# Kernel optimization log

Measured on AMD Instinct MI355X. Metric: run time of the kernel, lower is better.

Reference implementation:

```python
import jax, jax.numpy as jnp
import numpy as np

B, L, DIM = 8, 512, 8          # batch, seq len, raw channels (value dim D = 2*DIM = 16)
ET, HID, H = 128, 128, 2       # embed_time, hidden_size, num_heads
MAXLEN = 512
NEG = -1e9


def setup_inputs() -> dict:
    key = jax.random.key(0)
    ks = jax.random.split(key, 40)
    def n(i, shape, s=0.05):
        return jax.random.normal(ks[i], shape, jnp.float32) * s
    vals = jax.random.normal(ks[0], (B, L, DIM), jnp.float32)
    msk = (jax.random.uniform(ks[1], (B, L, DIM)) > 0.2).astype(jnp.float32)
    x = jnp.concatenate([vals, msk], -1)                      # (B, L, 2*DIM)
    time_steps = jax.random.uniform(ks[2], (B, L), jnp.float32)
    return {
        'x': x, 'time_steps': time_steps,
        # learned time embedding: Linear(1, ET-1) periodic + Linear(1,1)
        'w_per': n(3, (1, ET - 1)), 'b_per': n(4, (ET - 1,)),
        'w_lin': n(5, (1, 1)), 'b_lin': n(6, (1,)),
        # MultiTimeAttention projections
        'Wq_t': n(7, (ET, ET)), 'bq_t': n(8, (ET,)),
        'Wk_t': n(9, (ET, ET)), 'bk_t': n(10, (ET,)),
        'Wo_t': n(11, (2 * DIM * H, HID)), 'bo_t': n(12, (HID,)),
        'pos_emb': n(13, (MAXLEN + 1, HID)), 'cls_emb': n(14, (1, HID)),
        # transformer block (BERT-style post-LN encoder layer, d_ff=HID)
        'tWq': n(15, (HID, HID)), 'tbq': n(16, (HID,)),
        'tWk': n(17, (HID, HID)), 'tbk': n(18, (HID,)),
        'tWv': n(19, (HID, HID)), 'tbv': n(20, (HID,)),
        'tWo': n(21, (HID, HID)), 'tbo': n(22, (HID,)),
        'ln1_g': jnp.ones((HID,), jnp.float32), 'ln1_b': jnp.zeros((HID,), jnp.float32),
        'fW1': n(23, (HID, HID)), 'fb1': n(24, (HID,)),
        'fW2': n(25, (HID, HID)), 'fb2': n(26, (HID,)),
        'ln2_g': jnp.ones((HID,), jnp.float32), 'ln2_b': jnp.zeros((HID,), jnp.float32),
        # BertPooler
        'pW': n(27, (HID, HID)), 'pb': n(28, (HID,)),
    }


def _time_emb(tt, w_per, b_per, w_lin, b_lin):
    tt = tt[..., None]                                        # (B, L, 1)
    return jnp.concatenate([tt @ w_lin + b_lin, jnp.sin(tt @ w_per + b_per)], -1)


def _ln(x, g, b, eps=1e-5):
    m = x.mean(-1, keepdims=True)
    v = ((x - m) ** 2).mean(-1, keepdims=True)
    return (x - m) / jnp.sqrt(v + eps) * g + b


def _mta(q_emb, k_emb, value, mask, Wq, bq, Wk, bk, Wo, bo):
    # MultiTimeAttention: scores broadcast to value-channel axis, softmax over keys
    D = value.shape[-1]
    dk = ET // H
    def split(e, W, b):
        p = e @ W + b
        return p.reshape(e.shape[0], -1, H, dk).transpose(0, 2, 1, 3)
    q = split(q_emb, Wq, bq)                                  # (Bq, H, Lq, dk)
    k = split(k_emb, Wk, bk)                                  # (B,  H, Lk, dk)
    scores = jnp.matmul(q, k.swapaxes(-1, -2)) / jnp.sqrt(jnp.float32(dk))  # (B,H,Lq,Lk)
    s5 = jnp.where(mask[:, None, None, :, :] == 0, NEG, scores[..., None])  # (B,H,Lq,Lk,D)
    p = jax.nn.softmax(s5, axis=-2)
    out = jnp.einsum('bhqkd,bkd->bhqd', p, value)             # (B, H, Lq, D)
    Bv = value.shape[0]
    out = out.transpose(0, 2, 1, 3).reshape(Bv, -1, H * D)
    return out @ Wo + bo


def _tblock(x, tWq, tbq, tWk, tbk, tWv, tbv, tWo, tbo, ln1_g, ln1_b,
            fW1, fb1, fW2, fb2, ln2_g, ln2_b):
    Bq, Lq, _ = x.shape
    dk = HID // H
    def heads(W, b):
        return (x @ W + b).reshape(Bq, Lq, H, dk).transpose(0, 2, 1, 3)
    q, k, v = heads(tWq, tbq), heads(tWk, tbk), heads(tWv, tbv)
    a = jax.nn.softmax(jnp.matmul(q, k.swapaxes(-1, -2)) / jnp.sqrt(jnp.float32(dk)), -1)
    o = jnp.matmul(a, v).transpose(0, 2, 1, 3).reshape(Bq, Lq, HID) @ tWo + tbo
    x = _ln(x + o, ln1_g, ln1_b)
    f = jax.nn.relu(x @ fW1 + fb1) @ fW2 + fb2
    return _ln(x + f, ln2_g, ln2_b)


def reference(x, time_steps, w_per, b_per, w_lin, b_lin,
              Wq_t, bq_t, Wk_t, bk_t, Wo_t, bo_t, pos_emb, cls_emb,
              tWq, tbq, tWk, tbk, tWv, tbv, tWo, tbo, ln1_g, ln1_b,
              fW1, fb1, fW2, fb2, ln2_g, ln2_b, pW, pb):
    Bx = x.shape[0]
    mask_half = x[:, :, DIM:]
    mask = jnp.concatenate([mask_half, mask_half], -1)        # (B, L, 2*DIM)
    key_e = _time_emb(time_steps, w_per, b_per, w_lin, b_lin)
    tq_e = _time_emb(time_steps, w_per, b_per, w_lin, b_lin)  # query_time_steps=None -> same
    cls_t = jnp.linspace(0.0, 1.0, 128, dtype=jnp.float32)[None]
    cls_q_e = _time_emb(cls_t, w_per, b_per, w_lin, b_lin)    # (1, 128, ET)
    cls_out = _mta(cls_q_e, key_e, x, mask, Wq_t, bq_t, Wk_t, bk_t, Wo_t, bo_t)
    out = _mta(tq_e, key_e, x, mask, Wq_t, bq_t, Wk_t, bk_t, Wo_t, bo_t)
    tb = (tWq, tbq, tWk, tbk, tWv, tbv, tWo, tbo, ln1_g, ln1_b,
          fW1, fb1, fW2, fb2, ln2_g, ln2_b)
    cls_repr = jnp.broadcast_to(cls_emb[None, :, :], (Bx, 1, HID))
    # encode(cls_out, is_pooling=True), pooling='bert': no pos emb, take token 0
    h = _tblock(jnp.concatenate([cls_repr, cls_out], 1), *tb)
    cls_pooling = jnp.tanh(h[:, 0] @ pW + pb)                 # (B, HID)
    # encode(out, is_pooling=False) [pretrain path]: pos emb + transformer, drop CLS
    h2 = jnp.concatenate([cls_repr, out], 1)                  # (B, L+1, HID)
    h2 = h2 + pos_emb[:h2.shape[1]][None]
    h2 = _tblock(h2, *tb)
    last_hidden_state = h2[:, 1:]                             # (B, L, HID)
    return cls_pooling, last_hidden_state
```

## Files before the change

### kernel.cpp

```cpp
#include <hip/hip_runtime.h>
#include <hip/hip_bf16.h>
#include <math.h>


static constexpr int NM_ = 8 * 513;
static constexpr int NC_ = 8 * 129;
static constexpr int NT_ = NM_ + NC_;

using bf = __hip_bfloat16;
typedef __attribute__((ext_vector_type(8))) short bf16x8;
typedef __attribute__((ext_vector_type(4))) short bf16x4;
typedef __attribute__((ext_vector_type(4))) float floatx4;
typedef __attribute__((ext_vector_type(8))) unsigned short ushortx8;

__device__ __forceinline__ float wave_reduce_sum(float v) {
    #pragma unroll
    for (int off = 32; off >= 1; off >>= 1) v += __shfl_xor(v, off);
    return v;
}
__device__ __forceinline__ float wave_reduce_max(float v) {
    #pragma unroll
    for (int off = 32; off >= 1; off >>= 1) v = fmaxf(v, __shfl_xor(v, off));
    return v;
}
__device__ __forceinline__ float u2f(unsigned short u) {
    return __uint_as_float(((unsigned)u) << 16);
}
__device__ __forceinline__ unsigned short f2u(float f) {
    unsigned u = __float_as_uint(f);
    return (unsigned short)((u + 0x7FFF + ((u >> 16) & 1)) >> 16);
}
__device__ __forceinline__ bf16x8 join8(bf16x4 lo, bf16x4 hi) {
    return __builtin_shufflevector(lo, hi, 0, 1, 2, 3, 4, 5, 6, 7);
}
__device__ __forceinline__ float rdin(const void* p, int i, int flag) {
    return flag ? u2f(((const unsigned short*)p)[i]) : ((const float*)p)[i];
}

struct PrepAll {
    const void* src[32]; int n[32]; int dstoff[32];
    const void* wsrc[8]; unsigned short* wdst[8]; float wscale[8];
    const void* ts; const void* w_per; const void* b_per;
    const void* w_lin; const void* b_lin;
    unsigned short* key_e16;
    const unsigned short* det;
};
__global__ void prep_all_kernel(PrepAll a, float* dst) {
    int flag = (a.det[0] == 0x3F80u) ? 1 : 0;
    int blk = blockIdx.x, tid = threadIdx.x;
    if (blk < 8224) {
        int which = blk / 257, bi = blk - which * 257;
        int i = bi * 256 + tid;
        if (i < a.n[which]) dst[a.dstoff[which] + i] = rdin(a.src[which], i, flag);
    } else if (blk < 8736) {
        int p = blk - 8224;
        int m = p >> 6;
        int idx = (p & 63) * 256 + tid;
        int c = idx >> 9;
        int l = (idx >> 3) & 63;
        int j = idx & 7;
        int k = (c >> 3) * 32 + (l >> 4) * 8 + j;
        int n = (c & 7) * 16 + (l & 15);
        a.wdst[m][idx] = f2u(rdin(a.wsrc[m], k * 128 + n, flag) * a.wscale[m]);
    } else {
        int p = blk - 8736;
        int row = p * 2 + (tid >> 7), j = tid & 127;
        float t = (row < 4096) ? rdin(a.ts, row, flag)
                               : (float)(row - 4096) * (1.0f / 127.0f);
        float v;
        if (j == 0) v = t * rdin(a.w_lin, 0, flag) + rdin(a.b_lin, 0, flag);
        else        v = sinf(t * rdin(a.w_per, j - 1, flag) + rdin(a.b_per, j - 1, flag));
        a.key_e16[row * 128 + j] = f2u(v);
    }
}

struct GemmM {
    const void* A[3]; const unsigned short* W[3]; const float* bias[3];
    unsigned short* C[3];
    int M[3]; int act[3]; int abf[3]; float bscale[3];
};
__global__ void __launch_bounds__(256)
gemm_mfma_kernel(GemmM p) {
    int y = blockIdx.y;
    const unsigned short* Wsw = p.W[y];
    const float* bias = p.bias[y];
    unsigned short* C = p.C[y];
    int M = p.M[y], act = p.act[y], abf = p.abf[y];
    float bscale = p.bscale[y];
    int m0 = blockIdx.x * 16;
    if (m0 >= M) return;
    __shared__ unsigned short As[16][136];
    int tid = threadIdx.x;
    if (abf) {
        const unsigned short* A = (const unsigned short*)p.A[y];
        int r = tid >> 4, c0 = (tid & 15) * 8;
        ushortx8 v = {0, 0, 0, 0, 0, 0, 0, 0};
        if (m0 + r < M) v = *(const ushortx8*)(A + (size_t)(m0 + r) * 128 + c0);
        *(ushortx8*)&As[r][c0] = v;
    } else {
        const float* A = (const float*)p.A[y];
        int r = tid >> 4, c0 = (tid & 15) * 8;
        float4 v0 = make_float4(0.f, 0.f, 0.f, 0.f), v1 = v0;
        if (m0 + r < M) {
            v0 = *(const float4*)(A + (size_t)(m0 + r) * 128 + c0);
            v1 = *(const float4*)(A + (size_t)(m0 + r) * 128 + c0 + 4);
        }
        *(ushort4*)&As[r][c0] = make_ushort4(f2u(v0.x), f2u(v0.y), f2u(v0.z), f2u(v0.w));
        *(ushort4*)&As[r][c0 + 4] = make_ushort4(f2u(v1.x), f2u(v1.y), f2u(v1.z), f2u(v1.w));
    }
    __syncthreads();

    int wv = tid >> 6, lane = tid & 63;
    floatx4 acc0 = {0.f, 0.f, 0.f, 0.f}, acc1 = acc0;
    int am = lane & 15, aq = lane >> 4;
    #pragma unroll
    for (int ks = 0; ks < 4; ++ks) {
        bf16x8 af = *(bf16x8*)&As[am][ks * 32 + aq * 8];
        const unsigned short* base = Wsw + ((size_t)ks * 8 + 2 * wv) * 512 + lane * 8;
        bf16x8 b0 = *(const bf16x8*)(base);
        bf16x8 b1 = *(const bf16x8*)(base + 512);
        acc0 = __builtin_amdgcn_mfma_f32_16x16x32_bf16(af, b0, acc0, 0, 0, 0);
        acc1 = __builtin_amdgcn_mfma_f32_16x16x32_bf16(af, b1, acc1, 0, 0, 0);
    }
    int col = lane & 15, rowb = (lane >> 4) * 4;
    #pragma unroll
    for (int t = 0; t < 2; ++t) {
        floatx4 acc = t ? acc1 : acc0;
        int n = wv * 32 + t * 16 + col;
        float bv = bias[n] * bscale;
        #pragma unroll
        for (int rg = 0; rg < 4; ++rg) {
            int m = m0 + rowb + rg;
            if (m < M) {
                float o = acc[rg] + bv;
                if (act) o = fmaxf(o, 0.f);
                C[(size_t)m * 128 + n] = f2u(o);
            }
        }
    }
}

__global__ void __launch_bounds__(256)
gemm_mfma_ln_kernel(const unsigned short* A, const unsigned short* Wsw, const float* bias,
                    const float* resid, const float* gam, const float* bet,
                    float* C) {
    int m0 = blockIdx.x * 16;
    __shared__ unsigned short As[16][136];
    __shared__ float redS[4][4][4], redQ[4][4][4];
    __shared__ float smean[16], sinv[16];
    int tid = threadIdx.x;
    {
        int r = tid >> 4, c0 = (tid & 15) * 8;
        ushortx8 v = *(const ushortx8*)(A + (size_t)(m0 + r) * 128 + c0);
        *(ushortx8*)&As[r][c0] = v;
    }
    __syncthreads();

    int wv = tid >> 6, lane = tid & 63;
    floatx4 acc0 = {0.f, 0.f, 0.f, 0.f}, acc1 = acc0;
    int am = lane & 15, aq = lane >> 4;
    #pragma unroll
    for (int ks = 0; ks < 4; ++ks) {
        bf16x8 af = *(bf16x8*)&As[am][ks * 32 + aq * 8];
        const unsigned short* base = Wsw + ((size_t)ks * 8 + 2 * wv) * 512 + lane * 8;
        bf16x8 b0 = *(const bf16x8*)(base);
        bf16x8 b1 = *(const bf16x8*)(base + 512);
        acc0 = __builtin_amdgcn_mfma_f32_16x16x32_bf16(af, b0, acc0, 0, 0, 0);
        acc1 = __builtin_amdgcn_mfma_f32_16x16x32_bf16(af, b1, acc1, 0, 0, 0);
    }

    int col = lane & 15, g = lane >> 4, rowb = g * 4;
    float ov[2][4];
    #pragma unroll
    for (int t = 0; t < 2; ++t) {
        int n = wv * 32 + t * 16 + col;
        float bv = bias[n];
        floatx4 acc = t ? acc1 : acc0;
        #pragma unroll
        for (int rg = 0; rg < 4; ++rg)
            ov[t][rg] = acc[rg] + bv + resid[(size_t)(m0 + rowb + rg) * 128 + n];
    }
    #pragma unroll
    for (int rg = 0; rg < 4; ++rg) {
        float s = ov[0][rg] + ov[1][rg];
        float q = ov[0][rg] * ov[0][rg] + ov[1][rg] * ov[1][rg];
        #pragma unroll
        for (int off = 8; off >= 1; off >>= 1) {
            s += __shfl_xor(s, off);
            q += __shfl_xor(q, off);
        }
        if ((lane & 15) == 0) { redS[wv][g][rg] = s; redQ[wv][g][rg] = q; }
    }
    __syncthreads();
    if (tid < 16) {
        int gg = tid >> 2, rg = tid & 3;
        float s = redS[0][gg][rg] + redS[1][gg][rg] + redS[2][gg][rg] + redS[3][gg][rg];
        float q = redQ[0][gg][rg] + redQ[1][gg][rg] + redQ[2][gg][rg] + redQ[3][gg][rg];
        float mean = s * 0.0078125f;
        float var = q * 0.0078125f - mean * mean;
        smean[tid] = mean;
        sinv[tid] = rsqrtf(var + 1e-5f);
    }
    __syncthreads();
    #pragma unroll
    for (int t = 0; t < 2; ++t) {
        int n = wv * 32 + t * 16 + col;
        float gm = gam[n], bb = bet[n];
        #pragma unroll
        for (int rg = 0; rg < 4; ++rg) {
            int row = rowb + rg;
            C[(size_t)(m0 + row) * 128 + n] = (ov[t][rg] - smean[row]) * sinv[row] * gm + bb;
        }
    }
}

__global__ void __launch_bounds__(256)
ffn_ln_kernel(const float* x1, const unsigned short* W1, const float* b1,
              const unsigned short* W2, const float* b2,
              const float* gam, const float* bet, float* C) {
    int m0 = blockIdx.x * 16;
    __shared__ float Xs[16][128];
    __shared__ unsigned short As[16][136];
    __shared__ unsigned short Hs[16][136];
    __shared__ float redS[4][4][4], redQ[4][4][4];
    __shared__ float smean[16], sinv[16];
    int tid = threadIdx.x;
    {
        int r = tid >> 4, c0 = (tid & 15) * 8;
        float4 v0 = *(const float4*)(x1 + (size_t)(m0 + r) * 128 + c0);
        float4 v1 = *(const float4*)(x1 + (size_t)(m0 + r) * 128 + c0 + 4);
        *(float4*)&Xs[r][c0] = v0;
        *(float4*)&Xs[r][c0 + 4] = v1;
        *(ushort4*)&As[r][c0] = make_ushort4(f2u(v0.x), f2u(v0.y), f2u(v0.z), f2u(v0.w));
        *(ushort4*)&As[r][c0 + 4] = make_ushort4(f2u(v1.x), f2u(v1.y), f2u(v1.z), f2u(v1.w));
    }
    __syncthreads();

    int wv = tid >> 6, lane = tid & 63;
    int am = lane & 15, aq = lane >> 4;
    int col = lane & 15, g = lane >> 4, rowb = g * 4;

    {
        floatx4 acc0 = {0.f, 0.f, 0.f, 0.f}, acc1 = acc0;
        #pragma unroll
        for (int ks = 0; ks < 4; ++ks) {
            bf16x8 af = *(bf16x8*)&As[am][ks * 32 + aq * 8];
            const unsigned short* base = W1 + ((size_t)ks * 8 + 2 * wv) * 512 + lane * 8;
            bf16x8 bb0 = *(const bf16x8*)(base);
            bf16x8 bb1 = *(const bf16x8*)(base + 512);
            acc0 = __builtin_amdgcn_mfma_f32_16x16x32_bf16(af, bb0, acc0, 0, 0, 0);
            acc1 = __builtin_amdgcn_mfma_f32_16x16x32_bf16(af, bb1, acc1, 0, 0, 0);
        }
        #pragma unroll
        for (int t = 0; t < 2; ++t) {
            int n = wv * 32 + t * 16 + col;
            float bv = b1[n];
            floatx4 acc = t ? acc1 : acc0;
            #pragma unroll
            for (int rg = 0; rg < 4; ++rg)
                Hs[rowb + rg][n] = f2u(fmaxf(acc[rg] + bv, 0.f));
        }
    }
    __syncthreads();

    floatx4 acc0 = {0.f, 0.f, 0.f, 0.f}, acc1 = acc0;
    #pragma unroll
    for (int ks = 0; ks < 4; ++ks) {
        bf16x8 af = *(bf16x8*)&Hs[am][ks * 32 + aq * 8];
        const unsigned short* base = W2 + ((size_t)ks * 8 + 2 * wv) * 512 + lane * 8;
        bf16x8 bb0 = *(const bf16x8*)(base);
        bf16x8 bb1 = *(const bf16x8*)(base + 512);
        acc0 = __builtin_amdgcn_mfma_f32_16x16x32_bf16(af, bb0, acc0, 0, 0, 0);
        acc1 = __builtin_amdgcn_mfma_f32_16x16x32_bf16(af, bb1, acc1, 0, 0, 0);
    }
    float ov[2][4];
    #pragma unroll
    for (int t = 0; t < 2; ++t) {
        int n = wv * 32 + t * 16 + col;
        float bv = b2[n];
        floatx4 acc = t ? acc1 : acc0;
        #pragma unroll
        for (int rg = 0; rg < 4; ++rg)
            ov[t][rg] = acc[rg] + bv + Xs[rowb + rg][n];
    }
    #pragma unroll
    for (int rg = 0; rg < 4; ++rg) {
        float s = ov[0][rg] + ov[1][rg];
        float q = ov[0][rg] * ov[0][rg] + ov[1][rg] * ov[1][rg];
        #pragma unroll
        for (int off = 8; off >= 1; off >>= 1) {
            s += __shfl_xor(s, off);
            q += __shfl_xor(q, off);
        }
        if ((lane & 15) == 0) { redS[wv][g][rg] = s; redQ[wv][g][rg] = q; }
    }
    __syncthreads();
    if (tid < 16) {
        int gg = tid >> 2, rg = tid & 3;
        float s = redS[0][gg][rg] + redS[1][gg][rg] + redS[2][gg][rg] + redS[3][gg][rg];
        float q = redQ[0][gg][rg] + redQ[1][gg][rg] + redQ[2][gg][rg] + redQ[3][gg][rg];
        float mean = s * 0.0078125f;
        float var = q * 0.0078125f - mean * mean;
        smean[tid] = mean;
        sinv[tid] = rsqrtf(var + 1e-5f);
    }
    __syncthreads();
    #pragma unroll
    for (int t = 0; t < 2; ++t) {
        int n = wv * 32 + t * 16 + col;
        float gm = gam[n], bb = bet[n];
        #pragma unroll
        for (int rg = 0; rg < 4; ++rg) {
            int row = rowb + rg;
            C[(size_t)(m0 + row) * 128 + n] = (ov[t][rg] - smean[row]) * sinv[row] * gm + bb;
        }
    }
}

__global__ void mta_out_assemble_kernel(const float* att, const float* W, const float* bias,
                                        const float* cls_emb, const float* pos, float* xin) {
    int tid = threadIdx.x;
    if (blockIdx.x == 320) {
        for (int e = tid; e < 16 * 128; e += 256) {
            int i = e >> 7, j = e & 127;
            int b = i >> 1;
            if ((i & 1) == 0) xin[(size_t)(b * 513) * 128 + j] = cls_emb[j] + pos[j];
            else              xin[(size_t)(4104 + b * 129) * 128 + j] = cls_emb[j];
        }
        return;
    }
    int m0 = blockIdx.x * 16;
    __shared__ float As[16][36];
    int r = tid >> 4, gq = tid & 15, c0 = gq * 8;
    if (gq < 2) {
        const float* src = att + (size_t)(m0 + r) * 32 + gq * 16;
        *(float4*)&As[r][gq * 16]      = *(const float4*)(src);
        *(float4*)&As[r][gq * 16 + 4]  = *(const float4*)(src + 4);
        *(float4*)&As[r][gq * 16 + 8]  = *(const float4*)(src + 8);
        *(float4*)&As[r][gq * 16 + 12] = *(const float4*)(src + 12);
    }
    __syncthreads();
    float acc[8];
    #pragma unroll
    for (int j = 0; j < 8; ++j) acc[j] = bias[c0 + j];
    #pragma unroll 8
    for (int k = 0; k < 32; ++k) {
        float a = As[r][k];
        const float4 w0 = *(const float4*)(W + (size_t)k * 128 + c0);
        const float4 w1 = *(const float4*)(W + (size_t)k * 128 + c0 + 4);
        acc[0] = fmaf(a, w0.x, acc[0]); acc[1] = fmaf(a, w0.y, acc[1]);
        acc[2] = fmaf(a, w0.z, acc[2]); acc[3] = fmaf(a, w0.w, acc[3]);
        acc[4] = fmaf(a, w1.x, acc[4]); acc[5] = fmaf(a, w1.y, acc[5]);
        acc[6] = fmaf(a, w1.z, acc[6]); acc[7] = fmaf(a, w1.w, acc[7]);
    }
    int m = m0 + r;
    size_t dstrow;
    if (m < 1024) {
        int b = m >> 7, rr = m & 127;
        dstrow = (size_t)(4104 + b * 129 + 1 + rr);
    } else {
        int mm = m - 1024;
        int b = mm >> 9, rr = mm & 511;
        dstrow = (size_t)(b * 513 + 1 + rr);
        const float* pr = pos + (size_t)(1 + rr) * 128 + c0;
        float4 p0 = *(const float4*)(pr);
        float4 p1 = *(const float4*)(pr + 4);
        acc[0] += p0.x; acc[1] += p0.y; acc[2] += p0.z; acc[3] += p0.w;
        acc[4] += p1.x; acc[5] += p1.y; acc[6] += p1.z; acc[7] += p1.w;
    }
    *(float4*)(xin + dstrow * 128 + c0) = make_float4(acc[0], acc[1], acc[2], acc[3]);
    *(float4*)(xin + dstrow * 128 + c0 + 4) = make_float4(acc[4], acc[5], acc[6], acc[7]);
}

__global__ void __launch_bounds__(256)
mta_att_kernel(const unsigned short* qp_cls, const unsigned short* qp_main,
               const unsigned short* kp, const float* x,
               float* att_cls, float* att_mn) {
    int is_cls = (blockIdx.x >= 32);
    int qt = is_cls ? (blockIdx.x - 32) : blockIdx.x;
    int h = blockIdx.y, b = blockIdx.z;
    int tid = threadIdx.x, lane = tid & 63, wv = tid >> 6;
    __shared__ unsigned short Qs[16][72];
    __shared__ unsigned short KV[64][72];
    __shared__ unsigned short sp[16][520];
    float* xv = (float*)&KV[0][0];
    int q0 = qt * 16;

    if (tid < 128) {
        int r = tid >> 3, c0 = (tid & 7) * 8;
        const unsigned short* qrow = is_cls ? (qp_cls + (size_t)(q0 + r) * 128 + h * 64)
                                            : (qp_main + (size_t)(b * 512 + q0 + r) * 128 + h * 64);
        *(ushortx8*)&Qs[r][c0] = *(const ushortx8*)(qrow + c0);
    }
    __syncthreads();

    bf16x8 qf0, qf1;
    {
        int m = lane & 15, g = lane >> 4;
        qf0 = *(const bf16x8*)&Qs[m][g * 8];
        qf1 = *(const bf16x8*)&Qs[m][32 + g * 8];
    }

    for (int kt = 0; kt < 8; ++kt) {
        int k0 = kt * 64;
        {
            int kk = tid >> 3, e0 = (tid & 7) * 8;
            #pragma unroll
            for (int it = 0; it < 2; ++it, kk += 32)
                *(ushortx8*)&KV[kk][e0] =
                    *(const ushortx8*)(kp + (size_t)(b * 512 + k0 + kk) * 128 + h * 64 + e0);
        }
        __syncthreads();
        int kn = lane & 15, g = lane >> 4;
        floatx4 acc = {0.f, 0.f, 0.f, 0.f};
        {
            bf16x8 b0 = *(const bf16x8*)&KV[wv * 16 + kn][g * 8];
            acc = __builtin_amdgcn_mfma_f32_16x16x32_bf16(qf0, b0, acc, 0, 0, 0);
            bf16x8 b1 = *(const bf16x8*)&KV[wv * 16 + kn][32 + g * 8];
            acc = __builtin_amdgcn_mfma_f32_16x16x32_bf16(qf1, b1, acc, 0, 0, 0);
        }
        int colk = k0 + wv * 16 + kn;
        #pragma unroll
        for (int rg = 0; rg < 4; ++rg) sp[g * 4 + rg][colk] = f2u(acc[rg]);
        __syncthreads();
    }

    for (int rr = wv; rr < 16; rr += 4) {
        float m = -1e30f;
        for (int k = lane; k < 512; k += 64) m = fmaxf(m, u2f(sp[rr][k]));
        m = wave_reduce_max(m);
        for (int k = lane; k < 512; k += 64) sp[rr][k] = f2u(expf(u2f(sp[rr][k]) - m));
    }

    int d = lane >> 3, sub = lane & 7;
    int qb = wv * 4;
    float num[4] = {0.f, 0.f, 0.f, 0.f}, den[4] = {0.f, 0.f, 0.f, 0.f};
    for (int kt = 0; kt < 8; ++kt) {
        int k0 = kt * 64;
        __syncthreads();
        {
            int kk = tid >> 2, c0 = (tid & 3) * 4;
            float4 v = *(const float4*)(x + (size_t)(b * 512 + k0 + kk) * 16 + c0);
            xv[kk * 17 + c0] = v.x; xv[kk * 17 + c0 + 1] = v.y;
            xv[kk * 17 + c0 + 2] = v.z; xv[kk * 17 + c0 + 3] = v.w;
        }
        __syncthreads();
        #pragma unroll
        for (int i = 0; i < 8; ++i) {
            int kk = sub + 8 * i;
            float mk = xv[kk * 17 + 8 + d];
            float vv = xv[kk * 17 + d];
            #pragma unroll
            for (int q = 0; q < 4; ++q) {
                float em = u2f(sp[qb + q][k0 + kk]) * mk;
                den[q] += em;
                num[q] = fmaf(em, vv, num[q]);
            }
        }
    }
    #pragma unroll
    for (int q = 0; q < 4; ++q) {
        #pragma unroll
        for (int off2 = 4; off2 >= 1; off2 >>= 1) {
            num[q] += __shfl_xor(num[q], off2);
            den[q] += __shfl_xor(den[q], off2);
        }
        if (sub == 0) {
            int row = q0 + qb + q;
            float* dst = is_cls ? (att_cls + (size_t)(b * 128 + row) * 32)
                                : (att_mn + (size_t)(b * 512 + row) * 32);
            dst[h * 16 + d] = num[q] / den[q];
            dst[h * 16 + 8 + d] = 1.0f;
        }
    }
}

__global__ void __launch_bounds__(256)
tb_att_kernel(const unsigned short* qp, const unsigned short* kp,
              const unsigned short* vp, unsigned short* outp) {
    int is_cls = (blockIdx.x >= 33);
    int qt = is_cls ? blockIdx.x - 33 : blockIdx.x;
    int h = blockIdx.y, b = blockIdx.z;
    int Lq = is_cls ? 129 : 513;
    int base = is_cls ? (4104 + b * 129) : (b * 513);
    int nkt = is_cls ? 3 : 9;
    int tid = threadIdx.x, lane = tid & 63, wv = tid >> 6;
    __shared__ unsigned short Qs[16][72];
    __shared__ unsigned short KV[64][72];
    __shared__ unsigned short sp[16][588];
    __shared__ float rinv[16];
    int q0 = qt * 16;

    if (tid < 128) {
        int r = tid >> 3, c0 = (tid & 7) * 8;
        int qr = q0 + r;
        ushortx8 v = {0, 0, 0, 0, 0, 0, 0, 0};
        if (qr < Lq) v = *(const ushortx8*)(qp + (size_t)(base + qr) * 128 + h * 64 + c0);
        *(ushortx8*)&Qs[r][c0] = v;
    }
    __syncthreads();

    bf16x8 qf0, qf1;
    {
        int m = lane & 15, g = lane >> 4;
        qf0 = *(const bf16x8*)&Qs[m][g * 8];
        qf1 = *(const bf16x8*)&Qs[m][32 + g * 8];
    }

    for (int kt = 0; kt < nkt; ++kt) {
        int k0 = kt * 64;
        {
            int kk = tid >> 3, e0 = (tid & 7) * 8;
            #pragma unroll
            for (int it = 0; it < 2; ++it, kk += 32) {
                int krow = k0 + kk;
                ushortx8 v = {0, 0, 0, 0, 0, 0, 0, 0};
                if (krow < Lq) v = *(const ushortx8*)(kp + (size_t)(base + krow) * 128 + h * 64 + e0);
                *(ushortx8*)&KV[kk][e0] = v;
            }
        }
        __syncthreads();
        int kn = lane & 15, g = lane >> 4;
        floatx4 acc = {0.f, 0.f, 0.f, 0.f};
        {
            bf16x8 b0 = *(const bf16x8*)&KV[wv * 16 + kn][g * 8];
            acc = __builtin_amdgcn_mfma_f32_16x16x32_bf16(qf0, b0, acc, 0, 0, 0);
            bf16x8 b1 = *(const bf16x8*)&KV[wv * 16 + kn][32 + g * 8];
            acc = __builtin_amdgcn_mfma_f32_16x16x32_bf16(qf1, b1, acc, 0, 0, 0);
        }
        int colk = k0 + wv * 16 + kn;
        #pragma unroll
        for (int rg = 0; rg < 4; ++rg)
            sp[g * 4 + rg][colk] = f2u((colk < Lq) ? acc[rg] : -1e30f);
        __syncthreads();
    }

    int kend = nkt * 64;
    for (int rr = wv; rr < 16; rr += 4) {
        float m = -1e30f;
        for (int k = lane; k < kend; k += 64) m = fmaxf(m, u2f(sp[rr][k]));
        m = wave_reduce_max(m);
        float sum = 0.f;
        for (int k = lane; k < kend; k += 64) {
            float e = expf(u2f(sp[rr][k]) - m);
            sp[rr][k] = f2u(e);
            sum += e;
        }
        sum = wave_reduce_sum(sum);
        if (lane == 0) rinv[rr] = 1.f / sum;
    }

    floatx4 oacc = {0.f, 0.f, 0.f, 0.f};
    for (int kt = 0; kt < nkt; ++kt) {
        int k0 = kt * 64;
        __syncthreads();
        {
            int kk = tid & 31, e0 = (tid >> 5) * 8;
            #pragma unroll
            for (int it = 0; it < 2; ++it, kk += 32) {
                int krow = k0 + kk;
                ushortx8 v = {0, 0, 0, 0, 0, 0, 0, 0};
                if (krow < Lq) v = *(const ushortx8*)(vp + (size_t)(base + krow) * 128 + h * 64 + e0);
                #pragma unroll
                for (int j = 0; j < 8; ++j) KV[e0 + j][kk] = v[j];
            }
        }
        __syncthreads();
        int dn = lane & 15, g = lane >> 4;
        #pragma unroll
        for (int c = 0; c < 2; ++c) {
            bf16x4 plo = *(const bf16x4*)&sp[lane & 15][k0 + c * 32 + g * 8];
            bf16x4 phi = *(const bf16x4*)&sp[lane & 15][k0 + c * 32 + g * 8 + 4];
            bf16x8 vf = *(const bf16x8*)&KV[wv * 16 + dn][c * 32 + g * 8];
            oacc = __builtin_amdgcn_mfma_f32_16x16x32_bf16(join8(plo, phi), vf, oacc, 0, 0, 0);
        }
    }
    int dcol = wv * 16 + (lane & 15), g = lane >> 4;
    #pragma unroll
    for (int rg = 0; rg < 4; ++rg) {
        int q = g * 4 + rg;
        int qr = q0 + q;
        if (qr < Lq)
            outp[(size_t)(base + qr) * 128 + h * 64 + dcol] = f2u(oacc[rg] * rinv[q]);
    }
}

__global__ void pool_gemm_kernel(const float* A, int lda, const float* W, const float* bias,
                                 float* C) {
    __shared__ float As[8][132];
    int tid = threadIdx.x;
    int r = tid >> 5, g = tid & 31;
    for (int c = g; c < 128; c += 32) As[r][c] = A[(size_t)r * lda + c];
    __syncthreads();
    int rr = tid >> 5, c0 = (tid & 31) * 4;
    float acc[4];
    #pragma unroll
    for (int j = 0; j < 4; ++j) acc[j] = bias[c0 + j];
    for (int k = 0; k < 128; ++k) {
        float a = As[rr][k];
        const float4 w0 = *(const float4*)(W + (size_t)k * 128 + c0);
        acc[0] = fmaf(a, w0.x, acc[0]); acc[1] = fmaf(a, w0.y, acc[1]);
        acc[2] = fmaf(a, w0.z, acc[2]); acc[3] = fmaf(a, w0.w, acc[3]);
    }
    *(float4*)(C + (size_t)rr * 128 + c0) = make_float4(acc[0], acc[1], acc[2], acc[3]);
}

__global__ void finalize_kernel(const float* clsraw, const float* h2, float* out, int total) {
    int idx = blockIdx.x * 256 + threadIdx.x;
    if (idx >= total) return;
    float v;
    if (idx < 1024) {
        v = tanhf(clsraw[idx]);
    } else {
        int t = idx - 1024;
        int b = t >> 16;
        int rem = t & 65535;
        int i = rem >> 7, j = rem & 127;
        v = h2[((size_t)(b * 513 + 1 + i)) * 128 + j];
    }
    out[idx] = v;
}

extern "C" void kernel_launch(void* const* d_in, const int* in_sizes, int n_in,
                              void* d_out, int out_size, void* d_ws, size_t ws_size,
                              hipStream_t stream) {
    float* w = (float*)d_ws;
    size_t off = 0;
    auto alloc = [&](size_t n) {
        float* p = w + off;
        off += (n + 3) & ~(size_t)3;
        return p;
    };
    auto allocU = [&](size_t n) { return (unsigned short*)alloc((n + 1) / 2); };

    PrepAll pa{};
    int nn = n_in < 32 ? n_in : 32;
    float* fin[32];
    for (int i = 0; i < nn; ++i) {
        pa.src[i] = d_in[i];
        pa.n[i] = in_sizes[i];
        fin[i] = alloc(in_sizes[i]);
        pa.dstoff[i] = (int)(fin[i] - w);
    }
    for (int i = nn; i < 32; ++i) { pa.src[i] = nullptr; pa.n[i] = 0; pa.dstoff[i] = 0; }

    const float* x       = fin[0];
    const float* bq_t    = fin[7];
    const float* bk_t    = fin[9];
    const float* Wo_t    = fin[10]; const float* bo_t = fin[11];
    const float* pos_emb = fin[12]; const float* cls_emb = fin[13];
    const float* tbq = fin[15]; const float* tbk = fin[17]; const float* tbv = fin[19];
    const float* tbo = fin[21];
    const float* ln1_g = fin[22]; const float* ln1_b = fin[23];
    const float* fb1 = fin[25]; const float* fb2 = fin[27];
    const float* ln2_g = fin[28]; const float* ln2_b = fin[29];
    const float* pW = fin[30]; const float* pb = fin[31];

    const int widx[8] = {8, 6, 14, 16, 18, 20, 24, 26};
    unsigned short* wsw[8];
    for (int i = 0; i < 8; ++i) {
        wsw[i] = allocU(16384);
        pa.wsrc[i] = d_in[widx[i]];
        pa.wdst[i] = wsw[i];
        pa.wscale[i] = (i == 1 || i == 2) ? 0.125f : 1.0f;
    }
    pa.ts = d_in[1]; pa.w_per = d_in[2]; pa.b_per = d_in[3];
    pa.w_lin = d_in[4]; pa.b_lin = d_in[5];
    pa.det = (const unsigned short*)d_in[22];

    unsigned short* key_e16 = allocU(4224 * 128);
    unsigned short* cls_e16 = key_e16 + 4096 * 128;
    pa.key_e16 = key_e16;

    unsigned short* qp_main16 = allocU(4096 * 128);
    unsigned short* kp_main16 = allocU(4096 * 128);
    unsigned short* qp_cls16  = allocU(128 * 128);
    float* att_all = alloc(5120 * 32);
    float* att_cls = att_all;
    float* att_mn  = att_all + 1024 * 32;
    float* xin     = alloc((size_t)NT_ * 128);
    unsigned short* tbq16 = allocU((size_t)NT_ * 128);
    unsigned short* tbk16 = allocU((size_t)NT_ * 128);
    unsigned short* tbv16 = allocU((size_t)NT_ * 128);
    unsigned short* tba16 = allocU((size_t)NT_ * 128);
    float* tb_x1   = alloc((size_t)NT_ * 128);
    float* x2      = alloc((size_t)NT_ * 128);
    float* clsraw  = alloc(8 * 128);
    (void)ws_size;

    prep_all_kernel<<<10848, 256, 0, stream>>>(pa, w);

    {
        GemmM p{};
        p.A[0] = key_e16; p.W[0] = wsw[0]; p.bias[0] = bk_t; p.C[0] = kp_main16;
        p.M[0] = 4096; p.act[0] = 0; p.abf[0] = 1; p.bscale[0] = 1.f;
        p.A[1] = key_e16; p.W[1] = wsw[1]; p.bias[1] = bq_t; p.C[1] = qp_main16;
        p.M[1] = 4096; p.act[1] = 0; p.abf[1] = 1; p.bscale[1] = 0.125f;
        p.A[2] = cls_e16; p.W[2] = wsw[1]; p.bias[2] = bq_t; p.C[2] = qp_cls16;
        p.M[2] = 128; p.act[2] = 0; p.abf[2] = 1; p.bscale[2] = 0.125f;
        gemm_mfma_kernel<<<dim3(256, 3), 256, 0, stream>>>(p);
    }

    mta_att_kernel<<<dim3(40, 2, 8), 256, 0, stream>>>(qp_cls16, qp_main16, kp_main16,
                                                       x, att_cls, att_mn);

    mta_out_assemble_kernel<<<321, 256, 0, stream>>>(att_all, Wo_t, bo_t, cls_emb, pos_emb, xin);

    {
        GemmM p{};
        const unsigned short* Ws[3] = {wsw[2], wsw[3], wsw[4]};
        const float* bs[3] = {tbq, tbk, tbv};
        unsigned short* Cs[3] = {tbq16, tbk16, tbv16};
        float sc[3] = {0.125f, 1.f, 1.f};
        for (int y = 0; y < 3; ++y) {
            p.A[y] = xin; p.W[y] = Ws[y]; p.bias[y] = bs[y]; p.C[y] = Cs[y];
            p.M[y] = NT_; p.act[y] = 0; p.abf[y] = 0; p.bscale[y] = sc[y];
        }
        gemm_mfma_kernel<<<dim3((NT_ + 15) / 16, 3), 256, 0, stream>>>(p);
    }

    tb_att_kernel<<<dim3(42, 2, 8), 256, 0, stream>>>(tbq16, tbk16, tbv16, tba16);

    gemm_mfma_ln_kernel<<<NT_ / 16, 256, 0, stream>>>(tba16, wsw[5], tbo, xin, ln1_g, ln1_b, tb_x1);

    ffn_ln_kernel<<<NT_ / 16, 256, 0, stream>>>(tb_x1, wsw[6], fb1, wsw[7], fb2, ln2_g, ln2_b, x2);

    pool_gemm_kernel<<<1, 256, 0, stream>>>(x2 + (size_t)4104 * 128, 129 * 128, pW, pb, clsraw);

    finalize_kernel<<<(out_size + 255) / 256, 256, 0, stream>>>(clsraw, x2, (float*)d_out, out_size);
}
```

Measured before the change: 202.5 us.

## Fuse output scatter into FFN-LN, MFMA att-value reduction, skip unused input copies

The FFN+LayerNorm kernel now writes the last hidden state straight into the output buffer and stores only the CLS rows needed for pooling. The pooler applies tanh itself, so the finalize kernel and the full x2 buffer are dropped. The MTA attention value/mask weighted sum becomes a bf16 MFMA over a staged masked-value matrix instead of scalar loops with shuffles. The prep kernel also skips fp32 copies of inputs never read in fp32. Together this removes one launch and a large copy pass but lowers the precision of the attention numerator and denominator to bf16.

```diff
diff --git a/kernel.cpp b/kernel.cpp
--- a/kernel.cpp
+++ b/kernel.cpp
@@ -38,7 +38,7 @@
 }
 
 struct PrepAll {
-    const void* src[32]; int n[32]; int dstoff[32];
+    const void* src[32]; int n[32]; int dstoff[32]; int conv[32];
     const void* wsrc[8]; unsigned short* wdst[8]; float wscale[8];
     const void* ts; const void* w_per; const void* b_per;
     const void* w_lin; const void* b_lin;
@@ -50,6 +50,7 @@
     int blk = blockIdx.x, tid = threadIdx.x;
     if (blk < 8224) {
         int which = blk / 257, bi = blk - which * 257;
+        if (!a.conv[which]) return;
         int i = bi * 256 + tid;
         if (i < a.n[which]) dst[a.dstoff[which] + i] = rdin(a.src[which], i, flag);
     } else if (blk < 8736) {
@@ -217,7 +218,7 @@
 __global__ void __launch_bounds__(256)
 ffn_ln_kernel(const float* x1, const unsigned short* W1, const float* b1,
               const unsigned short* W2, const float* b2,
-              const float* gam, const float* bet, float* C) {
+              const float* gam, const float* bet, float* dout, float* x2c) {
     int m0 = blockIdx.x * 16;
     __shared__ float Xs[16][128];
     __shared__ unsigned short As[16][136];
@@ -312,7 +313,17 @@
         #pragma unroll
         for (int rg = 0; rg < 4; ++rg) {
             int row = rowb + rg;
-            C[(size_t)(m0 + row) * 128 + n] = (ov[t][rg] - smean[row]) * sinv[row] * gm + bb;
+            int m = m0 + row;
+            float val = (ov[t][rg] - smean[row]) * sinv[row] * gm + bb;
+            if (m < NM_) {
+                int b = m / 513, r = m - b * 513;
+                if (r >= 1)
+                    dout[1024 + (size_t)b * 65536 + (size_t)(r - 1) * 128 + n] = val;
+            } else {
+                int mc = m - NM_;
+                int b = mc / 129, r = mc - b * 129;
+                if (r == 0) x2c[b * 128 + n] = val;
+            }
         }
     }
 }
@@ -383,6 +394,7 @@
     __shared__ unsigned short Qs[16][72];
     __shared__ unsigned short KV[64][72];
     __shared__ unsigned short sp[16][520];
+    __shared__ unsigned short Bt[16][520];
     float* xv = (float*)&KV[0][0];
     int q0 = qt * 16;
 
@@ -432,9 +444,6 @@
         for (int k = lane; k < 512; k += 64) sp[rr][k] = f2u(expf(u2f(sp[rr][k]) - m));
     }
 
-    int d = lane >> 3, sub = lane & 7;
-    int qb = wv * 4;
-    float num[4] = {0.f, 0.f, 0.f, 0.f}, den[4] = {0.f, 0.f, 0.f, 0.f};
     for (int kt = 0; kt < 8; ++kt) {
         int k0 = kt * 64;
         __syncthreads();
@@ -445,33 +454,52 @@
             xv[kk * 17 + c0 + 2] = v.z; xv[kk * 17 + c0 + 3] = v.w;
         }
         __syncthreads();
-        #pragma unroll
-        for (int i = 0; i < 8; ++i) {
-            int kk = sub + 8 * i;
-            float mk = xv[kk * 17 + 8 + d];
-            float vv = xv[kk * 17 + d];
+        {
+            int c = tid & 15, k4 = (tid >> 4) * 4;
             #pragma unroll
-            for (int q = 0; q < 4; ++q) {
-                float em = u2f(sp[qb + q][k0 + kk]) * mk;
-                den[q] += em;
-                num[q] = fmaf(em, vv, num[q]);
+            for (int i = 0; i < 4; ++i) {
+                int k = k4 + i;
+                float val = (c < 8) ? xv[k * 17 + c] * xv[k * 17 + 8 + c]
+                                    : xv[k * 17 + c];
+                Bt[c][k0 + k] = f2u(val);
             }
         }
     }
-    #pragma unroll
-    for (int q = 0; q < 4; ++q) {
-        #pragma unroll
-        for (int off2 = 4; off2 >= 1; off2 >>= 1) {
-            num[q] += __shfl_xor(num[q], off2);
-            den[q] += __shfl_xor(den[q], off2);
-        }
-        if (sub == 0) {
-            int row = q0 + qb + q;
-            float* dst = is_cls ? (att_cls + (size_t)(b * 128 + row) * 32)
-                                : (att_mn + (size_t)(b * 512 + row) * 32);
-            dst[h * 16 + d] = num[q] / den[q];
-            dst[h * 16 + 8 + d] = 1.0f;
-        }
+    __syncthreads();
+
+    floatx4 macc = {0.f, 0.f, 0.f, 0.f};
+    {
+        int mq = lane & 15, g = lane >> 4;
+        #pragma unroll
+        for (int cc = 0; cc < 4; ++cc) {
+            int koff = (wv + cc * 4) * 32;
+            bf16x8 af = *(const bf16x8*)&sp[mq][koff + g * 8];
+            bf16x8 bfv = *(const bf16x8*)&Bt[mq][koff + g * 8];
+            macc = __builtin_amdgcn_mfma_f32_16x16x32_bf16(af, bfv, macc, 0, 0, 0);
+        }
+    }
+    float* redC = (float*)&KV[0][0];
+    float* Cfull = redC + 1024;
+    #pragma unroll
+    for (int rg = 0; rg < 4; ++rg) redC[(wv * 64 + lane) * 4 + rg] = macc[rg];
+    __syncthreads();
+    {
+        int l = tid >> 2, rg = tid & 3;
+        float s = redC[l * 4 + rg] + redC[(64 + l) * 4 + rg]
+                + redC[(128 + l) * 4 + rg] + redC[(192 + l) * 4 + rg];
+        int row = (l >> 4) * 4 + rg, c = l & 15;
+        Cfull[row * 16 + c] = s;
+    }
+    __syncthreads();
+    if (tid < 128) {
+        int r = tid >> 3, c = tid & 7;
+        float num = Cfull[r * 16 + c];
+        float den = Cfull[r * 16 + 8 + c];
+        int row = q0 + r;
+        float* dst = is_cls ? (att_cls + (size_t)(b * 128 + row) * 32)
+                            : (att_mn + (size_t)(b * 512 + row) * 32);
+        dst[h * 16 + c] = num / den;
+        dst[h * 16 + 8 + c] = 1.0f;
     }
 }
 
@@ -585,12 +613,12 @@
     }
 }
 
-__global__ void pool_gemm_kernel(const float* A, int lda, const float* W, const float* bias,
-                                 float* C) {
+__global__ void pool_tanh_kernel(const float* x2c, const float* W, const float* bias,
+                                 float* dout) {
     __shared__ float As[8][132];
     int tid = threadIdx.x;
     int r = tid >> 5, g = tid & 31;
-    for (int c = g; c < 128; c += 32) As[r][c] = A[(size_t)r * lda + c];
+    for (int c = g; c < 128; c += 32) As[r][c] = x2c[(size_t)r * 128 + c];
     __syncthreads();
     int rr = tid >> 5, c0 = (tid & 31) * 4;
     float acc[4];
@@ -602,23 +630,8 @@
         acc[0] = fmaf(a, w0.x, acc[0]); acc[1] = fmaf(a, w0.y, acc[1]);
         acc[2] = fmaf(a, w0.z, acc[2]); acc[3] = fmaf(a, w0.w, acc[3]);
     }
-    *(float4*)(C + (size_t)rr * 128 + c0) = make_float4(acc[0], acc[1], acc[2], acc[3]);
-}
-
-__global__ void finalize_kernel(const float* clsraw, const float* h2, float* out, int total) {
-    int idx = blockIdx.x * 256 + threadIdx.x;
-    if (idx >= total) return;
-    float v;
-    if (idx < 1024) {
-        v = tanhf(clsraw[idx]);
-    } else {
-        int t = idx - 1024;
-        int b = t >> 16;
-        int rem = t & 65535;
-        int i = rem >> 7, j = rem & 127;
-        v = h2[((size_t)(b * 513 + 1 + i)) * 128 + j];
-    }
-    out[idx] = v;
+    *(float4*)(dout + (size_t)rr * 128 + c0) =
+        make_float4(tanhf(acc[0]), tanhf(acc[1]), tanhf(acc[2]), tanhf(acc[3]));
 }
 
 extern "C" void kernel_launch(void* const* d_in, const int* in_sizes, int n_in,
@@ -636,13 +649,16 @@
     PrepAll pa{};
     int nn = n_in < 32 ? n_in : 32;
     float* fin[32];
+    const int needconv[32] = {1,0,0,0,0,0, 0,1, 0,1, 1,1, 1,1, 0,1, 0,1, 0,1,
+                              0,1, 1,1, 0,1, 0,1, 1,1, 1,1};
     for (int i = 0; i < nn; ++i) {
         pa.src[i] = d_in[i];
         pa.n[i] = in_sizes[i];
         fin[i] = alloc(in_sizes[i]);
         pa.dstoff[i] = (int)(fin[i] - w);
-    }
-    for (int i = nn; i < 32; ++i) { pa.src[i] = nullptr; pa.n[i] = 0; pa.dstoff[i] = 0; }
+        pa.conv[i] = needconv[i];
+    }
+    for (int i = nn; i < 32; ++i) { pa.src[i] = nullptr; pa.n[i] = 0; pa.dstoff[i] = 0; pa.conv[i] = 0; }
 
     const float* x       = fin[0];
     const float* bq_t    = fin[7];
@@ -684,9 +700,10 @@
     unsigned short* tbv16 = allocU((size_t)NT_ * 128);
     unsigned short* tba16 = allocU((size_t)NT_ * 128);
     float* tb_x1   = alloc((size_t)NT_ * 128);
-    float* x2      = alloc((size_t)NT_ * 128);
-    float* clsraw  = alloc(8 * 128);
+    float* x2c     = alloc(8 * 128);
     (void)ws_size;
+
+    float* outf = (float*)d_out;
 
     prep_all_kernel<<<10848, 256, 0, stream>>>(pa, w);
 
@@ -723,9 +740,8 @@
 
     gemm_mfma_ln_kernel<<<NT_ / 16, 256, 0, stream>>>(tba16, wsw[5], tbo, xin, ln1_g, ln1_b, tb_x1);
 
-    ffn_ln_kernel<<<NT_ / 16, 256, 0, stream>>>(tb_x1, wsw[6], fb1, wsw[7], fb2, ln2_g, ln2_b, x2);
-
-    pool_gemm_kernel<<<1, 256, 0, stream>>>(x2 + (size_t)4104 * 128, 129 * 128, pW, pb, clsraw);
-
-    finalize_kernel<<<(out_size + 255) / 256, 256, 0, stream>>>(clsraw, x2, (float*)d_out, out_size);
-}
+    ffn_ln_kernel<<<NT_ / 16, 256, 0, stream>>>(tb_x1, wsw[6], fb1, wsw[7], fb2,
+                                                ln2_g, ln2_b, outf, x2c);
+
+    pool_tanh_kernel<<<1, 256, 0, stream>>>(x2c, pW, pb, outf);
+}
```

New measurement: 197.3 us. 1.03x faster.
